# Optimization experiments

Hardware: AMD Instinct MI355X
Metric: run time of the kernel (lower is better)

## Reference

```python
import jax, jax.numpy as jnp
import numpy as np

N = 50000      # nodes (single node type)
E = 500000     # edges per relation
DIN = 128
DOUT = 128
NREL = 3


def setup_inputs() -> dict:
    key = jax.random.key(0)
    ks = jax.random.split(key, 16)
    inp = {"x": jax.random.normal(ks[0], (N, DIN), dtype=jnp.float32)}
    for i in range(NREL):
        inp[f"src_r{i}"] = jax.random.randint(ks[1 + 2 * i], (E,), 0, N)
        inp[f"dst_r{i}"] = jax.random.randint(ks[2 + 2 * i], (E,), 0, N)
    s = 1.0 / np.sqrt(DIN)  # nn.Linear default init range
    for i in range(NREL):
        inp[f"W_r{i}"] = jax.random.uniform(ks[7 + i], (DIN, DOUT), jnp.float32, -s, s)
    inp["W_loop"] = jax.random.uniform(ks[10], (DIN, DOUT), jnp.float32, -s, s)
    inp["b_loop"] = jnp.zeros((DOUT,), dtype=jnp.float32)
    return inp


def _rel_conv(x, src, dst, W):
    # DGL GraphConv(norm='right', weight=W, bias=False):
    # sum messages from src into dst, divide by in-degree (clamped to 1),
    # then apply the relation weight (aggregate-first since in_feat == out_feat).
    agg = jax.ops.segment_sum(x[src], dst, num_segments=N)            # [N, DIN]
    deg = jax.ops.segment_sum(jnp.ones_like(dst, dtype=x.dtype), dst,
                              num_segments=N)                          # [N]
    deg = jnp.clip(deg, 1.0, None)
    return (agg / deg[:, None]) @ W                                    # [N, DOUT]


def reference(x, src_r0, dst_r0, src_r1, dst_r1, src_r2, dst_r2,
              W_r0, W_r1, W_r2, W_loop, b_loop):
    # HeteroGraphConv: per-relation GraphConv, summed over relations sharing dst type
    h = (_rel_conv(x, src_r0, dst_r0, W_r0)
         + _rel_conv(x, src_r1, dst_r1, W_r1)
         + _rel_conv(x, src_r2, dst_r2, W_r2))
    # self-loop linear + activation (dropout=0.0 -> identity)
    h = h + x @ W_loop + b_loop
    return jax.nn.relu(h)
```

## Files before the change

kernel.cpp:

```cpp
#include <hip/hip_runtime.h>
#include <hip/hip_bf16.h>

#define N_NODES 50000
#define E_EDGES 500000
#define NREL    3
#define DIN     128
#define DOUT    128
#define SLOT    40
#define NB      782
#define BM      64
#define KB      8
#define CAP     1024
#define BUFW    16
#define NCHUNK  170

typedef __attribute__((ext_vector_type(8))) short bf16x8;
typedef __attribute__((ext_vector_type(4))) float f32x4;

__device__ __forceinline__ unsigned int f2bf(float f) {
    unsigned int u = __float_as_uint(f);
    unsigned int r = (u + 0x7FFFu + ((u >> 16) & 1u)) >> 16;
    return r;
}
__device__ __forceinline__ float bf2f_lo(unsigned int u) { return __uint_as_float(u << 16); }
__device__ __forceinline__ float bf2f_hi(unsigned int u) { return __uint_as_float(u & 0xFFFF0000u); }

__global__ __launch_bounds__(256) void k_binfill(const int* __restrict__ src0,
                                                 const int* __restrict__ dst0,
                                                 const int* __restrict__ src1,
                                                 const int* __restrict__ dst1,
                                                 const int* __restrict__ src2,
                                                 const int* __restrict__ dst2,
                                                 int* __restrict__ gcnt,
                                                 unsigned int* __restrict__ bins) {
    __shared__ unsigned int buf[NB][BUFW];
    __shared__ int cnt[NB];
    __shared__ int flushed[NB];

    const int tid   = threadIdx.x;
    const int rel   = blockIdx.x / NCHUNK;
    const int chunk = blockIdx.x % NCHUNK;
    const int EPB   = (E_EDGES + NCHUNK - 1) / NCHUNK;
    const int base  = chunk * EPB;
    const int eend  = min(base + EPB, E_EDGES);

    const int* srcp = (rel == 0) ? src0 : (rel == 1) ? src1 : src2;
    const int* dstp = (rel == 0) ? dst0 : (rel == 1) ? dst1 : dst2;

    for (int b = tid; b < NB; b += 256) { cnt[b] = 0; flushed[b] = 0; }
    __syncthreads();

    for (int it = base; it < eend; it += 256) {
        int e = it + tid;
        if (e < eend) {
            int d = dstp[e];
            int s = srcp[e];
            int bin = d >> 6;
            unsigned int entry = ((unsigned int)s << 6) | (unsigned int)(d & 63);
            int pos = atomicAdd(&cnt[bin], 1);
            if (pos - flushed[bin] < BUFW) {
                buf[bin][pos & (BUFW - 1)] = entry;
            } else {
                int g = atomicAdd(&gcnt[rel * NB + bin], 1);
                if (g < CAP) bins[(size_t)(rel * NB + bin) * CAP + g] = entry;
            }
        }
        __syncthreads();
        for (int b = tid; b < NB; b += 256) {
            while (cnt[b] - flushed[b] >= BUFW) {
                int f = flushed[b];
                int g = atomicAdd(&gcnt[rel * NB + b], BUFW);
                unsigned int* gp = bins + (size_t)(rel * NB + b) * CAP;
#pragma unroll
                for (int i = 0; i < BUFW; ++i) {
                    if (g + i < CAP) gp[g + i] = buf[b][(f + i) & (BUFW - 1)];
                }
                flushed[b] = f + BUFW;
            }
        }
        __syncthreads();
    }
    for (int b = tid; b < NB; b += 256) {
        int c = cnt[b], f = flushed[b];
        if (c > f) {
            int n = c - f;
            int g = atomicAdd(&gcnt[rel * NB + b], n);
            unsigned int* gp = bins + (size_t)(rel * NB + b) * CAP;
            for (int i = 0; i < n; ++i)
                if (g + i < CAP) gp[g + i] = buf[b][(f + i) & (BUFW - 1)];
        }
    }
}

__global__ __launch_bounds__(256) void k_xcast(const float* __restrict__ x,
                                               unsigned short* __restrict__ xb) {
    int i = (blockIdx.x * 256 + threadIdx.x) * 8;
    if (i >= N_NODES * DIN) return;
    float4 a = *reinterpret_cast<const float4*>(x + i);
    float4 b = *reinterpret_cast<const float4*>(x + i + 4);
    uint4 o;
    o.x = f2bf(a.x) | (f2bf(a.y) << 16);
    o.y = f2bf(a.z) | (f2bf(a.w) << 16);
    o.z = f2bf(b.x) | (f2bf(b.y) << 16);
    o.w = f2bf(b.z) | (f2bf(b.w) << 16);
    *reinterpret_cast<uint4*>(xb + i) = o;
}

__global__ __launch_bounds__(256) void k_wcast(const float* __restrict__ W0,
                                               const float* __restrict__ W1,
                                               const float* __restrict__ W2,
                                               const float* __restrict__ Wl,
                                               unsigned short* __restrict__ Wtb) {
    int t = blockIdx.x * 256 + threadIdx.x;
    if (t >= 4 * DIN * DOUT) return;
    int k   = t & 127;
    int c   = (t >> 7) & 127;
    int rel = t >> 14;
    const float* W = (rel == 0) ? W0 : (rel == 1) ? W1 : (rel == 2) ? W2 : Wl;
    Wtb[t] = (unsigned short)f2bf(W[(size_t)k * DOUT + c]);
}

__global__ __launch_bounds__(256) void k_gather(const unsigned short* __restrict__ xb,
                                                const int* __restrict__ gcnt,
                                                const unsigned int* __restrict__ bins,
                                                unsigned short* __restrict__ aggb) {
    __shared__ unsigned short lists[BM][SLOT];
    __shared__ int dcnt[BM];

    const int rel   = blockIdx.x / NB;
    const int blk   = blockIdx.x % NB;
    const int mbase = blk * BM;
    const int tid   = threadIdx.x;
    const int wave  = tid >> 6;
    const int lane  = tid & 63;
    const int g     = lane >> 4;
    const int li    = lane & 15;

    if (tid < BM) dcnt[tid] = 0;
    __syncthreads();

    const int bin = rel * NB + blk;
    const int n   = min(gcnt[bin], CAP);
    const unsigned int* bp = bins + (size_t)bin * CAP;
    for (int i = tid; i < n; i += 256) {
        unsigned int e = bp[i];
        int lo = (int)(e & 63u);
        int s  = (int)(e >> 6);
        int pos = atomicAdd(&dcnt[lo], 1);
        if (pos < SLOT) lists[lo][pos] = (unsigned short)s;
    }
    __syncthreads();

#pragma unroll
    for (int t = 0; t < 4; ++t) {
        const int local = wave * 16 + g * 4 + t;
        const int node  = mbase + local;
        if (node >= N_NODES) continue;
        const int dtrue = dcnt[local];
        const int d = min(dtrue, SLOT);
        const unsigned short* sb = &lists[local][0];
        const unsigned short* xbb = xb + (size_t)li * 8;

        float acc[8];
#pragma unroll
        for (int k = 0; k < 8; ++k) acc[k] = 0.f;

        int i = 0;
        for (; i + 4 <= d; i += 4) {
            ushort4 s4 = *reinterpret_cast<const ushort4*>(sb + i);
            uint4 u0 = *reinterpret_cast<const uint4*>(xbb + (size_t)s4.x * DIN);
            uint4 u1 = *reinterpret_cast<const uint4*>(xbb + (size_t)s4.y * DIN);
            uint4 u2 = *reinterpret_cast<const uint4*>(xbb + (size_t)s4.z * DIN);
            uint4 u3 = *reinterpret_cast<const uint4*>(xbb + (size_t)s4.w * DIN);
            acc[0] += bf2f_lo(u0.x) + bf2f_lo(u1.x) + bf2f_lo(u2.x) + bf2f_lo(u3.x);
            acc[1] += bf2f_hi(u0.x) + bf2f_hi(u1.x) + bf2f_hi(u2.x) + bf2f_hi(u3.x);
            acc[2] += bf2f_lo(u0.y) + bf2f_lo(u1.y) + bf2f_lo(u2.y) + bf2f_lo(u3.y);
            acc[3] += bf2f_hi(u0.y) + bf2f_hi(u1.y) + bf2f_hi(u2.y) + bf2f_hi(u3.y);
            acc[4] += bf2f_lo(u0.z) + bf2f_lo(u1.z) + bf2f_lo(u2.z) + bf2f_lo(u3.z);
            acc[5] += bf2f_hi(u0.z) + bf2f_hi(u1.z) + bf2f_hi(u2.z) + bf2f_hi(u3.z);
            acc[6] += bf2f_lo(u0.w) + bf2f_lo(u1.w) + bf2f_lo(u2.w) + bf2f_lo(u3.w);
            acc[7] += bf2f_hi(u0.w) + bf2f_hi(u1.w) + bf2f_hi(u2.w) + bf2f_hi(u3.w);
        }
        for (; i < d; ++i) {
            uint4 u0 = *reinterpret_cast<const uint4*>(xbb + (size_t)sb[i] * DIN);
            acc[0] += bf2f_lo(u0.x); acc[1] += bf2f_hi(u0.x);
            acc[2] += bf2f_lo(u0.y); acc[3] += bf2f_hi(u0.y);
            acc[4] += bf2f_lo(u0.z); acc[5] += bf2f_hi(u0.z);
            acc[6] += bf2f_lo(u0.w); acc[7] += bf2f_hi(u0.w);
        }

        const float inv = 1.0f / (float)max(dtrue, 1);
        uint4 o;
        o.x = f2bf(acc[0] * inv) | (f2bf(acc[1] * inv) << 16);
        o.y = f2bf(acc[2] * inv) | (f2bf(acc[3] * inv) << 16);
        o.z = f2bf(acc[4] * inv) | (f2bf(acc[5] * inv) << 16);
        o.w = f2bf(acc[6] * inv) | (f2bf(acc[7] * inv) << 16);
        *reinterpret_cast<uint4*>(aggb + (size_t)(rel * N_NODES + node) * DIN + li * 8) = o;
    }
}

__global__ __launch_bounds__(256) void k_gemm_mfma(const unsigned short* __restrict__ xb,
                                                   const unsigned short* __restrict__ aggb,
                                                   const unsigned short* __restrict__ Wtb,
                                                   const float* __restrict__ bias,
                                                   float* __restrict__ out) {
    __shared__ unsigned short At[BM][136];
    __shared__ unsigned short Bt[DOUT][136];

    const int tid   = threadIdx.x;
    const int mbase = blockIdx.x * BM;
    const int w     = tid >> 6;
    const int l     = tid & 63;
    const int lr    = l & 15;
    const int lk    = l >> 4;

    f32x4 acc[8];
#pragma unroll
    for (int ct = 0; ct < 8; ++ct) acc[ct] = (f32x4){0.f, 0.f, 0.f, 0.f};

    for (int rel = 0; rel < 4; ++rel) {
        __syncthreads();

        const unsigned short* Asrc = (rel < 3) ? (aggb + (size_t)rel * N_NODES * DIN) : xb;
#pragma unroll
        for (int j = 0; j < 4; ++j) {
            int idx = tid + j * 256;
            int row = idx >> 4;
            int oct = idx & 15;
            int node = mbase + row;
            int nc = node < N_NODES ? node : N_NODES - 1;
            uint4 u = *reinterpret_cast<const uint4*>(Asrc + (size_t)nc * DIN + oct * 8);
            *reinterpret_cast<uint4*>(&At[row][oct * 8]) = u;
        }
        const unsigned short* Bsrc = Wtb + (size_t)rel * DIN * DOUT;
#pragma unroll
        for (int j = 0; j < 8; ++j) {
            int idx = tid + j * 256;
            int c   = idx >> 4;
            int oct = idx & 15;
            uint4 u = *reinterpret_cast<const uint4*>(Bsrc + (size_t)c * DIN + oct * 8);
            *reinterpret_cast<uint4*>(&Bt[c][oct * 8]) = u;
        }
        __syncthreads();

#pragma unroll
        for (int kc = 0; kc < 4; ++kc) {
            bf16x8 a = *reinterpret_cast<const bf16x8*>(&At[w * 16 + lr][kc * 32 + lk * 8]);
#pragma unroll
            for (int ct = 0; ct < 8; ++ct) {
                bf16x8 b = *reinterpret_cast<const bf16x8*>(&Bt[ct * 16 + lr][kc * 32 + lk * 8]);
                acc[ct] = __builtin_amdgcn_mfma_f32_16x16x32_bf16(a, b, acc[ct], 0, 0, 0);
            }
        }
    }

#pragma unroll
    for (int ct = 0; ct < 8; ++ct) {
        int col = ct * 16 + lr;
        float bv = bias[col];
#pragma unroll
        for (int r = 0; r < 4; ++r) {
            int row = mbase + w * 16 + lk * 4 + r;
            if (row < N_NODES)
                out[(size_t)row * DOUT + col] = fmaxf(acc[ct][r] + bv, 0.f);
        }
    }
}

__global__ __launch_bounds__(256) void k_fill_direct(const int* __restrict__ src0,
                                                     const int* __restrict__ dst0,
                                                     const int* __restrict__ src1,
                                                     const int* __restrict__ dst1,
                                                     const int* __restrict__ src2,
                                                     const int* __restrict__ dst2,
                                                     int* __restrict__ cur,
                                                     unsigned short* __restrict__ slots) {
    int e = blockIdx.x * 256 + threadIdx.x;
    if (e >= E_EDGES) return;
    int d0 = dst0[e];
    int p0 = atomicAdd(&cur[0 * N_NODES + d0], 1);
    if (p0 < SLOT) slots[(size_t)(0 * N_NODES + d0) * SLOT + p0] = (unsigned short)src0[e];
    int d1 = dst1[e];
    int p1 = atomicAdd(&cur[1 * N_NODES + d1], 1);
    if (p1 < SLOT) slots[(size_t)(1 * N_NODES + d1) * SLOT + p1] = (unsigned short)src1[e];
    int d2 = dst2[e];
    int p2 = atomicAdd(&cur[2 * N_NODES + d2], 1);
    if (p2 < SLOT) slots[(size_t)(2 * N_NODES + d2) * SLOT + p2] = (unsigned short)src2[e];
}

__global__ __launch_bounds__(256) void k_fused_fb(const float* __restrict__ x,
                                                  const int* __restrict__ cur,
                                                  const unsigned short* __restrict__ slots,
                                                  const float* __restrict__ W0,
                                                  const float* __restrict__ W1,
                                                  const float* __restrict__ W2,
                                                  const float* __restrict__ Wl,
                                                  const float* __restrict__ bias,
                                                  float* __restrict__ out) {
    __shared__ float Ag[BM][132];
    __shared__ float Bs[KB][DOUT];

    const int tid   = threadIdx.x;
    const int mbase = blockIdx.x * BM;
    const int wave  = tid >> 6;
    const int lane  = tid & 63;
    const int g     = lane >> 4;
    const int li    = lane & 15;
    const int rg    = tid >> 5;
    const int cg    = tid & 31;

    float acc[8][4];
#pragma unroll
    for (int i = 0; i < 8; ++i)
#pragma unroll
        for (int j = 0; j < 4; ++j) acc[i][j] = 0.f;

    for (int rel = 0; rel < 4; ++rel) {
        __syncthreads();
        if (rel < 3) {
#pragma unroll
            for (int t = 0; t < 4; ++t) {
                const int local = wave * 16 + g * 4 + t;
                const int node  = mbase + local;
                float aA0 = 0.f, aA1 = 0.f, aA2 = 0.f, aA3 = 0.f;
                float aB0 = 0.f, aB1 = 0.f, aB2 = 0.f, aB3 = 0.f;
                int dd = 0;
                if (node < N_NODES) {
                    const int seg = rel * N_NODES + node;
                    int dtrue = cur[seg];
                    int d = min(dtrue, SLOT);
                    dd = dtrue;
                    const unsigned short* sb = slots + (size_t)seg * SLOT;
                    const float* xbp = x + (size_t)li * 8;
                    int i = 0;
                    for (; i + 4 <= d; i += 4) {
                        ushort4 s4 = *reinterpret_cast<const ushort4*>(sb + i);
                        const float* q0 = xbp + (size_t)s4.x * DIN;
                        const float* q1 = xbp + (size_t)s4.y * DIN;
                        const float* q2 = xbp + (size_t)s4.z * DIN;
                        const float* q3 = xbp + (size_t)s4.w * DIN;
                        float4 u0 = *reinterpret_cast<const float4*>(q0);
                        float4 w0 = *reinterpret_cast<const float4*>(q0 + 4);
                        float4 u1 = *reinterpret_cast<const float4*>(q1);
                        float4 w1 = *reinterpret_cast<const float4*>(q1 + 4);
                        float4 u2 = *reinterpret_cast<const float4*>(q2);
                        float4 w2 = *reinterpret_cast<const float4*>(q2 + 4);
                        float4 u3 = *reinterpret_cast<const float4*>(q3);
                        float4 w3 = *reinterpret_cast<const float4*>(q3 + 4);
                        aA0 += (u0.x + u1.x) + (u2.x + u3.x);
                        aA1 += (u0.y + u1.y) + (u2.y + u3.y);
                        aA2 += (u0.z + u1.z) + (u2.z + u3.z);
                        aA3 += (u0.w + u1.w) + (u2.w + u3.w);
                        aB0 += (w0.x + w1.x) + (w2.x + w3.x);
                        aB1 += (w0.y + w1.y) + (w2.y + w3.y);
                        aB2 += (w0.z + w1.z) + (w2.z + w3.z);
                        aB3 += (w0.w + w1.w) + (w2.w + w3.w);
                    }
                    for (; i < d; ++i) {
                        int s0 = sb[i];
                        const float* q0 = xbp + (size_t)s0 * DIN;
                        float4 u0 = *reinterpret_cast<const float4*>(q0);
                        float4 w0 = *reinterpret_cast<const float4*>(q0 + 4);
                        aA0 += u0.x; aA1 += u0.y; aA2 += u0.z; aA3 += u0.w;
                        aB0 += w0.x; aB1 += w0.y; aB2 += w0.z; aB3 += w0.w;
                    }
                }
                const float sc = 1.0f / (float)max(dd, 1);
                *reinterpret_cast<float4*>(&Ag[local][li * 8]) =
                    make_float4(aA0 * sc, aA1 * sc, aA2 * sc, aA3 * sc);
                *reinterpret_cast<float4*>(&Ag[local][li * 8 + 4]) =
                    make_float4(aB0 * sc, aB1 * sc, aB2 * sc, aB3 * sc);
            }
        } else {
#pragma unroll
            for (int j = 0; j < 8; ++j) {
                int idx = tid + j * 256;
                int row = idx >> 5;
                int q   = idx & 31;
                int node = mbase + row;
                float4 v = make_float4(0.f, 0.f, 0.f, 0.f);
                if (node < N_NODES)
                    v = *reinterpret_cast<const float4*>(x + (size_t)node * DIN + q * 4);
                *reinterpret_cast<float4*>(&Ag[row][q * 4]) = v;
            }
        }
        __syncthreads();

        const float* W = (rel == 0) ? W0 : (rel == 1) ? W1 : (rel == 2) ? W2 : Wl;
        for (int kc = 0; kc < 16; ++kc) {
            {
                int kk = tid >> 5;
                int cq = tid & 31;
                float4 v = *reinterpret_cast<const float4*>(W + (size_t)(kc * KB + kk) * DOUT + cq * 4);
                *reinterpret_cast<float4*>(&Bs[kk][cq * 4]) = v;
            }
            __syncthreads();
#pragma unroll
            for (int k = 0; k < KB; ++k) {
                float a[8], bb[4];
#pragma unroll
                for (int i = 0; i < 8; ++i) a[i] = Ag[rg * 8 + i][kc * KB + k];
                *reinterpret_cast<float4*>(&bb[0]) = *reinterpret_cast<const float4*>(&Bs[k][cg * 4]);
#pragma unroll
                for (int i = 0; i < 8; ++i)
#pragma unroll
                    for (int j = 0; j < 4; ++j) acc[i][j] += a[i] * bb[j];
            }
            __syncthreads();
        }
    }

    float4 bv = *reinterpret_cast<const float4*>(bias + cg * 4);
#pragma unroll
    for (int i = 0; i < 8; ++i) {
        int node = mbase + rg * 8 + i;
        if (node < N_NODES) {
            float4 o;
            o.x = fmaxf(acc[i][0] + bv.x, 0.f);
            o.y = fmaxf(acc[i][1] + bv.y, 0.f);
            o.z = fmaxf(acc[i][2] + bv.z, 0.f);
            o.w = fmaxf(acc[i][3] + bv.w, 0.f);
            *reinterpret_cast<float4*>(out + (size_t)node * DOUT + cg * 4) = o;
        }
    }
}

extern "C" void kernel_launch(void* const* d_in, const int* in_sizes, int n_in,
                              void* d_out, int out_size, void* d_ws, size_t ws_size,
                              hipStream_t stream) {
    const float* x    = (const float*)d_in[0];
    const int* src0   = (const int*)d_in[1];
    const int* dst0   = (const int*)d_in[2];
    const int* src1   = (const int*)d_in[3];
    const int* dst1   = (const int*)d_in[4];
    const int* src2   = (const int*)d_in[5];
    const int* dst2   = (const int*)d_in[6];
    const float* W0   = (const float*)d_in[7];
    const float* W1   = (const float*)d_in[8];
    const float* W2   = (const float*)d_in[9];
    const float* Wl   = (const float*)d_in[10];
    const float* bias = (const float*)d_in[11];
    float* out        = (float*)d_out;

    const size_t r0 = ((size_t)NREL * N_NODES * sizeof(int) + 255) & ~(size_t)255;
    const size_t r1 = ((size_t)NREL * N_NODES * SLOT * sizeof(unsigned short) + 255) & ~(size_t)255;
    const size_t sz_xb   = ((size_t)N_NODES * DIN * sizeof(unsigned short) + 255) & ~(size_t)255;
    const size_t sz_aggb = ((size_t)NREL * N_NODES * DIN * sizeof(unsigned short) + 255) & ~(size_t)255;
    const size_t sz_wtb  = ((size_t)4 * DIN * DOUT * sizeof(unsigned short) + 255) & ~(size_t)255;

    char* p = (char*)d_ws;
    int* gcnt             = (int*)p;
    unsigned short* slots = (unsigned short*)(p + r0);
    unsigned int* bins    = (unsigned int*)(p + r0);
    unsigned short* xb    = (unsigned short*)(p + r0 + r1);
    unsigned short* aggb  = (unsigned short*)(p + r0 + r1 + sz_xb);
    unsigned short* Wtb   = (unsigned short*)(p + r0 + r1 + sz_xb + sz_aggb);
    const size_t need = r0 + r1 + sz_xb + sz_aggb + sz_wtb;

    if (ws_size >= need) {
        hipMemsetAsync(gcnt, 0, (size_t)NREL * NB * sizeof(int), stream);
        k_binfill<<<NREL * NCHUNK, 256, 0, stream>>>(src0, dst0, src1, dst1, src2, dst2,
                                                     gcnt, bins);
        k_xcast<<<(N_NODES * DIN / 8 + 255) / 256, 256, 0, stream>>>(x, xb);
        k_wcast<<<(4 * DIN * DOUT + 255) / 256, 256, 0, stream>>>(W0, W1, W2, Wl, Wtb);
        k_gather<<<NREL * NB, 256, 0, stream>>>(xb, gcnt, bins, aggb);
        k_gemm_mfma<<<NB, 256, 0, stream>>>(xb, aggb, Wtb, bias, out);
    } else {
        hipMemsetAsync(gcnt, 0, (size_t)NREL * N_NODES * sizeof(int), stream);
        const int eb = (E_EDGES + 255) / 256;
        k_fill_direct<<<eb, 256, 0, stream>>>(src0, dst0, src1, dst1, src2, dst2, gcnt, slots);
        k_fused_fb<<<NB, 256, 0, stream>>>(x, gcnt, slots, W0, W1, W2, Wl, bias, out);
    }
}
```

Baseline: 206.0 us.

## Fuse neighbor gather into MFMA GEMM kernel, dropping aggregate buffer

```diff
diff --git a/kernel.cpp b/kernel.cpp
--- a/kernel.cpp
+++ b/kernel.cpp
@@ -120,95 +120,20 @@
     Wtb[t] = (unsigned short)f2bf(W[(size_t)k * DOUT + c]);
 }
 
-__global__ __launch_bounds__(256) void k_gather(const unsigned short* __restrict__ xb,
-                                                const int* __restrict__ gcnt,
-                                                const unsigned int* __restrict__ bins,
-                                                unsigned short* __restrict__ aggb) {
+__global__ __launch_bounds__(256) void k_fused_mfma(const unsigned short* __restrict__ xb,
+                                                    const int* __restrict__ gcnt,
+                                                    const unsigned int* __restrict__ bins,
+                                                    const unsigned short* __restrict__ Wtb,
+                                                    const float* __restrict__ bias,
+                                                    float* __restrict__ out) {
+    __shared__ unsigned short At[BM][136];
+    __shared__ unsigned short Bt[DOUT][136];
     __shared__ unsigned short lists[BM][SLOT];
     __shared__ int dcnt[BM];
 
-    const int rel   = blockIdx.x / NB;
-    const int blk   = blockIdx.x % NB;
+    const int tid   = threadIdx.x;
+    const int blk   = blockIdx.x;
     const int mbase = blk * BM;
-    const int tid   = threadIdx.x;
-    const int wave  = tid >> 6;
-    const int lane  = tid & 63;
-    const int g     = lane >> 4;
-    const int li    = lane & 15;
-
-    if (tid < BM) dcnt[tid] = 0;
-    __syncthreads();
-
-    const int bin = rel * NB + blk;
-    const int n   = min(gcnt[bin], CAP);
-    const unsigned int* bp = bins + (size_t)bin * CAP;
-    for (int i = tid; i < n; i += 256) {
-        unsigned int e = bp[i];
-        int lo = (int)(e & 63u);
-        int s  = (int)(e >> 6);
-        int pos = atomicAdd(&dcnt[lo], 1);
-        if (pos < SLOT) lists[lo][pos] = (unsigned short)s;
-    }
-    __syncthreads();
-
-#pragma unroll
-    for (int t = 0; t < 4; ++t) {
-        const int local = wave * 16 + g * 4 + t;
-        const int node  = mbase + local;
-        if (node >= N_NODES) continue;
-        const int dtrue = dcnt[local];
-        const int d = min(dtrue, SLOT);
-        const unsigned short* sb = &lists[local][0];
-        const unsigned short* xbb = xb + (size_t)li * 8;
-
-        float acc[8];
-#pragma unroll
-        for (int k = 0; k < 8; ++k) acc[k] = 0.f;
-
-        int i = 0;
-        for (; i + 4 <= d; i += 4) {
-            ushort4 s4 = *reinterpret_cast<const ushort4*>(sb + i);
-            uint4 u0 = *reinterpret_cast<const uint4*>(xbb + (size_t)s4.x * DIN);
-            uint4 u1 = *reinterpret_cast<const uint4*>(xbb + (size_t)s4.y * DIN);
-            uint4 u2 = *reinterpret_cast<const uint4*>(xbb + (size_t)s4.z * DIN);
-            uint4 u3 = *reinterpret_cast<const uint4*>(xbb + (size_t)s4.w * DIN);
-            acc[0] += bf2f_lo(u0.x) + bf2f_lo(u1.x) + bf2f_lo(u2.x) + bf2f_lo(u3.x);
-            acc[1] += bf2f_hi(u0.x) + bf2f_hi(u1.x) + bf2f_hi(u2.x) + bf2f_hi(u3.x);
-            acc[2] += bf2f_lo(u0.y) + bf2f_lo(u1.y) + bf2f_lo(u2.y) + bf2f_lo(u3.y);
-            acc[3] += bf2f_hi(u0.y) + bf2f_hi(u1.y) + bf2f_hi(u2.y) + bf2f_hi(u3.y);
-            acc[4] += bf2f_lo(u0.z) + bf2f_lo(u1.z) + bf2f_lo(u2.z) + bf2f_lo(u3.z);
-            acc[5] += bf2f_hi(u0.z) + bf2f_hi(u1.z) + bf2f_hi(u2.z) + bf2f_hi(u3.z);
-            acc[6] += bf2f_lo(u0.w) + bf2f_lo(u1.w) + bf2f_lo(u2.w) + bf2f_lo(u3.w);
-            acc[7] += bf2f_hi(u0.w) + bf2f_hi(u1.w) + bf2f_hi(u2.w) + bf2f_hi(u3.w);
-        }
-        for (; i < d; ++i) {
-            uint4 u0 = *reinterpret_cast<const uint4*>(xbb + (size_t)sb[i] * DIN);
-            acc[0] += bf2f_lo(u0.x); acc[1] += bf2f_hi(u0.x);
-            acc[2] += bf2f_lo(u0.y); acc[3] += bf2f_hi(u0.y);
-            acc[4] += bf2f_lo(u0.z); acc[5] += bf2f_hi(u0.z);
-            acc[6] += bf2f_lo(u0.w); acc[7] += bf2f_hi(u0.w);
-        }
-
-        const float inv = 1.0f / (float)max(dtrue, 1);
-        uint4 o;
-        o.x = f2bf(acc[0] * inv) | (f2bf(acc[1] * inv) << 16);
-        o.y = f2bf(acc[2] * inv) | (f2bf(acc[3] * inv) << 16);
-        o.z = f2bf(acc[4] * inv) | (f2bf(acc[5] * inv) << 16);
-        o.w = f2bf(acc[6] * inv) | (f2bf(acc[7] * inv) << 16);
-        *reinterpret_cast<uint4*>(aggb + (size_t)(rel * N_NODES + node) * DIN + li * 8) = o;
-    }
-}
-
-__global__ __launch_bounds__(256) void k_gemm_mfma(const unsigned short* __restrict__ xb,
-                                                   const unsigned short* __restrict__ aggb,
-                                                   const unsigned short* __restrict__ Wtb,
-                                                   const float* __restrict__ bias,
-                                                   float* __restrict__ out) {
-    __shared__ unsigned short At[BM][136];
-    __shared__ unsigned short Bt[DOUT][136];
-
-    const int tid   = threadIdx.x;
-    const int mbase = blockIdx.x * BM;
     const int w     = tid >> 6;
     const int l     = tid & 63;
     const int lr    = l & 15;
@@ -221,17 +146,6 @@
     for (int rel = 0; rel < 4; ++rel) {
         __syncthreads();
 
-        const unsigned short* Asrc = (rel < 3) ? (aggb + (size_t)rel * N_NODES * DIN) : xb;
-#pragma unroll
-        for (int j = 0; j < 4; ++j) {
-            int idx = tid + j * 256;
-            int row = idx >> 4;
-            int oct = idx & 15;
-            int node = mbase + row;
-            int nc = node < N_NODES ? node : N_NODES - 1;
-            uint4 u = *reinterpret_cast<const uint4*>(Asrc + (size_t)nc * DIN + oct * 8);
-            *reinterpret_cast<uint4*>(&At[row][oct * 8]) = u;
-        }
         const unsigned short* Bsrc = Wtb + (size_t)rel * DIN * DOUT;
 #pragma unroll
         for (int j = 0; j < 8; ++j) {
@@ -241,7 +155,78 @@
             uint4 u = *reinterpret_cast<const uint4*>(Bsrc + (size_t)c * DIN + oct * 8);
             *reinterpret_cast<uint4*>(&Bt[c][oct * 8]) = u;
         }
-        __syncthreads();
+
+        if (rel < 3) {
+            if (tid < BM) dcnt[tid] = 0;
+            __syncthreads();
+
+            const int bin = rel * NB + blk;
+            const int n   = min(gcnt[bin], CAP);
+            const unsigned int* bp = bins + (size_t)bin * CAP;
+            for (int i = tid; i < n; i += 256) {
+                unsigned int e = bp[i];
+                int lo = (int)(e & 63u);
+                int s  = (int)(e >> 6);
+                int pos = atomicAdd(&dcnt[lo], 1);
+                if (pos < SLOT) lists[lo][pos] = (unsigned short)s;
+            }
+            __syncthreads();
+
+#pragma unroll
+            for (int t = 0; t < 4; ++t) {
+                const int local = w * 16 + lk * 4 + t;
+                const int dtrue = dcnt[local];
+                const int d = min(dtrue, SLOT);
+                const unsigned short* sb = &lists[local][0];
+                const unsigned short* xbb = xb + (size_t)lr * 8;
+
+                float a0 = 0.f, a1 = 0.f, a2 = 0.f, a3 = 0.f;
+                float a4 = 0.f, a5 = 0.f, a6 = 0.f, a7 = 0.f;
+                int i = 0;
+                for (; i + 4 <= d; i += 4) {
+                    ushort4 s4 = *reinterpret_cast<const ushort4*>(sb + i);
+                    uint4 u0 = *reinterpret_cast<const uint4*>(xbb + (size_t)s4.x * DIN);
+                    uint4 u1 = *reinterpret_cast<const uint4*>(xbb + (size_t)s4.y * DIN);
+                    uint4 u2 = *reinterpret_cast<const uint4*>(xbb + (size_t)s4.z * DIN);
+                    uint4 u3 = *reinterpret_cast<const uint4*>(xbb + (size_t)s4.w * DIN);
+                    a0 += bf2f_lo(u0.x) + bf2f_lo(u1.x) + bf2f_lo(u2.x) + bf2f_lo(u3.x);
+                    a1 += bf2f_hi(u0.x) + bf2f_hi(u1.x) + bf2f_hi(u2.x) + bf2f_hi(u3.x);
+                    a2 += bf2f_lo(u0.y) + bf2f_lo(u1.y) + bf2f_lo(u2.y) + bf2f_lo(u3.y);
+                    a3 += bf2f_hi(u0.y) + bf2f_hi(u1.y) + bf2f_hi(u2.y) + bf2f_hi(u3.y);
+                    a4 += bf2f_lo(u0.z) + bf2f_lo(u1.z) + bf2f_lo(u2.z) + bf2f_lo(u3.z);
+                    a5 += bf2f_hi(u0.z) + bf2f_hi(u1.z) + bf2f_hi(u2.z) + bf2f_hi(u3.z);
+                    a6 += bf2f_lo(u0.w) + bf2f_lo(u1.w) + bf2f_lo(u2.w) + bf2f_lo(u3.w);
+                    a7 += bf2f_hi(u0.w) + bf2f_hi(u1.w) + bf2f_hi(u2.w) + bf2f_hi(u3.w);
+                }
+                for (; i < d; ++i) {
+                    uint4 u0 = *reinterpret_cast<const uint4*>(xbb + (size_t)sb[i] * DIN);
+                    a0 += bf2f_lo(u0.x); a1 += bf2f_hi(u0.x);
+                    a2 += bf2f_lo(u0.y); a3 += bf2f_hi(u0.y);
+                    a4 += bf2f_lo(u0.z); a5 += bf2f_hi(u0.z);
+                    a6 += bf2f_lo(u0.w); a7 += bf2f_hi(u0.w);
+                }
+                const float inv = 1.0f / (float)max(dtrue, 1);
+                uint4 o;
+                o.x = f2bf(a0 * inv) | (f2bf(a1 * inv) << 16);
+                o.y = f2bf(a2 * inv) | (f2bf(a3 * inv) << 16);
+                o.z = f2bf(a4 * inv) | (f2bf(a5 * inv) << 16);
+                o.w = f2bf(a6 * inv) | (f2bf(a7 * inv) << 16);
+                *reinterpret_cast<uint4*>(&At[local][lr * 8]) = o;
+            }
+            __syncthreads();
+        } else {
+#pragma unroll
+            for (int j = 0; j < 4; ++j) {
+                int idx = tid + j * 256;
+                int row = idx >> 4;
+                int oct = idx & 15;
+                int node = mbase + row;
+                int nc = node < N_NODES ? node : N_NODES - 1;
+                uint4 u = *reinterpret_cast<const uint4*>(xb + (size_t)nc * DIN + oct * 8);
+                *reinterpret_cast<uint4*>(&At[row][oct * 8]) = u;
+            }
+            __syncthreads();
+        }
 
 #pragma unroll
         for (int kc = 0; kc < 4; ++kc) {
@@ -444,18 +429,16 @@
 
     const size_t r0 = ((size_t)NREL * N_NODES * sizeof(int) + 255) & ~(size_t)255;
     const size_t r1 = ((size_t)NREL * N_NODES * SLOT * sizeof(unsigned short) + 255) & ~(size_t)255;
-    const size_t sz_xb   = ((size_t)N_NODES * DIN * sizeof(unsigned short) + 255) & ~(size_t)255;
-    const size_t sz_aggb = ((size_t)NREL * N_NODES * DIN * sizeof(unsigned short) + 255) & ~(size_t)255;
-    const size_t sz_wtb  = ((size_t)4 * DIN * DOUT * sizeof(unsigned short) + 255) & ~(size_t)255;
+    const size_t sz_xb  = ((size_t)N_NODES * DIN * sizeof(unsigned short) + 255) & ~(size_t)255;
+    const size_t sz_wtb = ((size_t)4 * DIN * DOUT * sizeof(unsigned short) + 255) & ~(size_t)255;
 
     char* p = (char*)d_ws;
     int* gcnt             = (int*)p;
     unsigned short* slots = (unsigned short*)(p + r0);
     unsigned int* bins    = (unsigned int*)(p + r0);
     unsigned short* xb    = (unsigned short*)(p + r0 + r1);
-    unsigned short* aggb  = (unsigned short*)(p + r0 + r1 + sz_xb);
-    unsigned short* Wtb   = (unsigned short*)(p + r0 + r1 + sz_xb + sz_aggb);
-    const size_t need = r0 + r1 + sz_xb + sz_aggb + sz_wtb;
+    unsigned short* Wtb   = (unsigned short*)(p + r0 + r1 + sz_xb);
+    const size_t need = r0 + r1 + sz_xb + sz_wtb;
 
     if (ws_size >= need) {
         hipMemsetAsync(gcnt, 0, (size_t)NREL * NB * sizeof(int), stream);
@@ -463,8 +446,7 @@
                                                      gcnt, bins);
         k_xcast<<<(N_NODES * DIN / 8 + 255) / 256, 256, 0, stream>>>(x, xb);
         k_wcast<<<(4 * DIN * DOUT + 255) / 256, 256, 0, stream>>>(W0, W1, W2, Wl, Wtb);
-        k_gather<<<NREL * NB, 256, 0, stream>>>(xb, gcnt, bins, aggb);
-        k_gemm_mfma<<<NB, 256, 0, stream>>>(xb, aggb, Wtb, bias, out);
+        k_fused_mfma<<<NB, 256, 0, stream>>>(xb, gcnt, bins, Wtb, bias, out);
     } else {
         hipMemsetAsync(gcnt, 0, (size_t)NREL * N_NODES * sizeof(int), stream);
         const int eb = (E_EDGES + 255) / 256;
```

Result: slower. 227.4 us (+10.4%).
